# Optimization experiments

Hardware: AMD Instinct MI355X
Metric: run time of the kernel (lower is better)

Reference implementation:

```python
import jax, jax.numpy as jnp
import numpy as np

CH, G, K, STRIDE, RR = 256, 16, 7, 1, 4
GROUP = CH // G            # channels per group
PAD = (K - 1) // 2
BN_EPS = 1e-5


def setup_inputs() -> dict:
    key = jax.random.key(0)
    ks = jax.random.split(key, 9)
    b, dim = 16, 4096
    hid = CH // RR  # 64
    return {
        "x": jax.random.normal(ks[0], (b, CH, dim), jnp.float32),
        "w1": jax.random.normal(ks[1], (hid, CH), jnp.float32) * (1.0 / np.sqrt(CH)),
        "b1": jax.random.normal(ks[2], (hid,), jnp.float32) * 0.02,
        "bn_gamma": 1.0 + 0.1 * jax.random.normal(ks[3], (hid,), jnp.float32),
        "bn_beta": 0.1 * jax.random.normal(ks[4], (hid,), jnp.float32),
        "bn_mean": 0.1 * jax.random.normal(ks[5], (hid,), jnp.float32),
        "bn_var": jax.random.uniform(ks[6], (hid,), jnp.float32) + 0.5,
        "w2": jax.random.normal(ks[7], (K * G, hid), jnp.float32) * (1.0 / np.sqrt(hid)),
        "b2": jax.random.normal(ks[8], (K * G,), jnp.float32) * 0.02,
    }


def _involution(x, w1, b1, bn_gamma, bn_beta, bn_mean, bn_var, w2, b2):
    b, ch, dim = x.shape
    L = dim // STRIDE  # out_dim
    # unfold: pad then gather K shifted strided views -> [b, ch, K, L]
    xp = jnp.pad(x, ((0, 0), (0, 0), (PAD, PAD)))
    unfolded = jnp.stack(
        [xp[:, :, k : k + STRIDE * (L - 1) + 1 : STRIDE] for k in range(K)], axis=2
    )
    unfolded = unfolded.reshape(b, G, GROUP, K, L)
    # adaptive max pool to L (windows of size STRIDE); identity when STRIDE == 1
    pooled = x.reshape(b, ch, L, STRIDE).max(axis=-1)
    # kernel generator: 1x1 conv -> relu -> batchnorm (inference) -> 1x1 conv
    h = jnp.einsum("oc,bcl->bol", w1, pooled) + b1[:, None]
    h = jax.nn.relu(h)
    h = (h - bn_mean[:, None]) * jax.lax.rsqrt(bn_var[:, None] + BN_EPS)
    h = h * bn_gamma[:, None] + bn_beta[:, None]
    kern = jnp.einsum("oc,bcl->bol", w2, h) + b2[:, None]  # [b, K*G, L]
    kern = kern.reshape(b, G, K, L)
    # per-location dynamic kernel multiply + reduce over K
    out = jnp.einsum("bgkl,bgckl->bgcl", kern, unfolded)
    return out.reshape(b, ch, L)


def reference(x, w1, b1, bn_gamma, bn_beta, bn_mean, bn_var, w2, b2):
    return _involution(x, w1, b1, bn_gamma, bn_beta, bn_mean, bn_var, w2, b2)
```

## Files before the change

kernel.cpp:

```cpp
#include <hip/hip_runtime.h>

#define BB   16
#define CHN  256
#define DIMN 4096
#define KK   7
#define PADK 3
#define HID  64
#define KGN  112
#define RP   56
#define TLC  128
#define NPAN 8
#define PCH  32
#define XSTD 66
#define HSTD 132
#define BN_EPS 1e-5f

typedef __fp16 half2_t __attribute__((ext_vector_type(2)));
typedef __fp16 half8   __attribute__((ext_vector_type(8)));
typedef float  f32x4   __attribute__((ext_vector_type(4)));

union U32H2 { unsigned int u; half2_t h; };

static __device__ __forceinline__ unsigned int packf(float a, float b) {
    U32H2 t; t.h = __builtin_amdgcn_cvt_pkrtz(a, b); return t.u;
}
static __device__ __forceinline__ half2_t ash2(unsigned int u) { U32H2 t; t.u = u; return t.h; }
static __device__ __forceinline__ __fp16 u16h(unsigned short u) {
    return __builtin_bit_cast(__fp16, u);
}
static __device__ __forceinline__ unsigned short hu16(__fp16 h) {
    return __builtin_bit_cast(unsigned short, h);
}

__global__ __launch_bounds__(256) void setup_k(
    const float* __restrict__ w1, const float* __restrict__ w2,
    const float* __restrict__ bn_gamma, const float* __restrict__ bn_beta,
    const float* __restrict__ bn_mean,  const float* __restrict__ bn_var,
    __fp16* __restrict__ w1f, __fp16* __restrict__ w2f,
    float* __restrict__ scb, float* __restrict__ shb) {
    int t = blockIdx.x * 256 + threadIdx.x;
    if (t < HID * CHN) w1f[t] = (__fp16)w1[t];
    if (t < KGN * HID) w2f[t] = (__fp16)w2[t];
    if (t < HID) {
        float s = bn_gamma[t] * rsqrtf(bn_var[t] + BN_EPS);
        scb[t] = s;
        shb[t] = bn_beta[t] - bn_mean[t] * s;
    }
}

__global__ __launch_bounds__(256) void kerngen_k(
    const float* __restrict__ x,
    const __fp16* __restrict__ w1f,
    const float* __restrict__ b1,
    const float* __restrict__ scb, const float* __restrict__ shb,
    const __fp16* __restrict__ w2f,
    const float* __restrict__ b2,
    unsigned int* __restrict__ kern) {
    __shared__ unsigned int   xs[2][PCH * XSTD];
    __shared__ unsigned short hs[HID * HSTD];

    const int t    = threadIdx.x;
    const int lr   = t & 15;
    const int lg   = (t >> 4) & 3;
    const int w    = t >> 6;
    const int b    = blockIdx.x >> 5;
    const int l0   = (blockIdx.x & 31) * TLC;
    const int colw = 32 * w;

    const int colq = t & 31;
    const int chl0 = t >> 5;

    const float* xg = x + (size_t)b * CHN * DIMN + l0 + 4 * colq;

    float4 pre[4];
#pragma unroll
    for (int i = 0; i < 4; ++i)
        pre[i] = *(const float4*)(xg + (size_t)(chl0 + 8 * i) * DIMN);
#pragma unroll
    for (int i = 0; i < 4; ++i) {
        uint2 v;
        v.x = packf(pre[i].x, pre[i].y);
        v.y = packf(pre[i].z, pre[i].w);
        *(uint2*)&xs[0][(chl0 + 8 * i) * XSTD + 2 * colq] = v;
    }
    __syncthreads();

    f32x4 acc[4][2];
#pragma unroll
    for (int of = 0; of < 4; ++of)
#pragma unroll
        for (int cf = 0; cf < 2; ++cf) acc[of][cf] = (f32x4){0.f, 0.f, 0.f, 0.f};

    for (int p = 0; p < NPAN; ++p) {
        if (p + 1 < NPAN) {
#pragma unroll
            for (int i = 0; i < 4; ++i)
                pre[i] = *(const float4*)(xg + (size_t)((p + 1) * PCH + chl0 + 8 * i) * DIMN);
        }
        const unsigned short* xb16 = (const unsigned short*)xs[p & 1];
        half8 bf0, bf1;
#pragma unroll
        for (int j = 0; j < 8; ++j) {
            bf0[j] = u16h(xb16[(8 * lg + j) * HSTD + colw + lr]);
            bf1[j] = u16h(xb16[(8 * lg + j) * HSTD + colw + 16 + lr]);
        }
#pragma unroll
        for (int of = 0; of < 4; ++of) {
            half8 af = *(const half8*)(w1f + (16 * of + lr) * CHN + PCH * p + 8 * lg);
            acc[of][0] = __builtin_amdgcn_mfma_f32_16x16x32_f16(af, bf0, acc[of][0], 0, 0, 0);
            acc[of][1] = __builtin_amdgcn_mfma_f32_16x16x32_f16(af, bf1, acc[of][1], 0, 0, 0);
        }
        if (p + 1 < NPAN) {
            __syncthreads();
#pragma unroll
            for (int i = 0; i < 4; ++i) {
                uint2 v;
                v.x = packf(pre[i].x, pre[i].y);
                v.y = packf(pre[i].z, pre[i].w);
                *(uint2*)&xs[(p + 1) & 1][(chl0 + 8 * i) * XSTD + 2 * colq] = v;
            }
            __syncthreads();
        }
    }

#pragma unroll
    for (int of = 0; of < 4; ++of) {
#pragma unroll
        for (int r = 0; r < 4; ++r) {
            const int o  = 16 * of + 4 * lg + r;
            const float bo = b1[o], sc = scb[o], sh = shb[o];
#pragma unroll
            for (int cf = 0; cf < 2; ++cf) {
                float hv = fmaxf(acc[of][cf][r] + bo, 0.f) * sc + sh;
                hs[o * HSTD + colw + 16 * cf + lr] = hu16((__fp16)hv);
            }
        }
    }

    f32x4 acc2[7][2];
#pragma unroll
    for (int rf = 0; rf < 7; ++rf)
#pragma unroll
        for (int cf = 0; cf < 2; ++cf) acc2[rf][cf] = (f32x4){0.f, 0.f, 0.f, 0.f};

#pragma unroll
    for (int ks = 0; ks < 2; ++ks) {
        half8 h0, h1;
#pragma unroll
        for (int j = 0; j < 8; ++j) {
            h0[j] = u16h(hs[(32 * ks + 8 * lg + j) * HSTD + colw + lr]);
            h1[j] = u16h(hs[(32 * ks + 8 * lg + j) * HSTD + colw + 16 + lr]);
        }
#pragma unroll
        for (int rf = 0; rf < 7; ++rf) {
            half8 af = *(const half8*)(w2f + (16 * rf + lr) * HID + 32 * ks + 8 * lg);
            acc2[rf][0] = __builtin_amdgcn_mfma_f32_16x16x32_f16(af, h0, acc2[rf][0], 0, 0, 0);
            acc2[rf][1] = __builtin_amdgcn_mfma_f32_16x16x32_f16(af, h1, acc2[rf][1], 0, 0, 0);
        }
    }

    unsigned int* kb = kern + (size_t)b * RP * DIMN + l0;
#pragma unroll
    for (int rf = 0; rf < 7; ++rf) {
#pragma unroll
        for (int cf = 0; cf < 2; ++cf) {
#pragma unroll
            for (int pp = 0; pp < 2; ++pp) {
                const int r0  = 16 * rf + 4 * lg + 2 * pp;
                const int col = colw + 16 * cf + lr;
                float k0 = acc2[rf][cf][2 * pp + 0] + b2[r0 + 0];
                float k1 = acc2[rf][cf][2 * pp + 1] + b2[r0 + 1];
                kb[(size_t)(r0 >> 1) * DIMN + col] = packf(k0, k1);
            }
        }
    }
}

template <int OFF>
static __device__ inline void extract_kv(const uint4 q[4], float kv[KK][4]) {
#pragma unroll
    for (int k = 0; k < KK; ++k) {
        const int kk = k + OFF;
        const int i  = kk >> 1;
        const int h  = kk & 1;
#pragma unroll
        for (int j = 0; j < 4; ++j) {
            unsigned int u = (&q[i].x)[j];
            half2_t hh = ash2(u);
            kv[k][j] = h ? (float)hh[1] : (float)hh[0];
        }
    }
}

__global__ __launch_bounds__(256) void involution_k(
    const float* __restrict__ x,
    const unsigned int* __restrict__ kern,
    float* __restrict__ out) {
    int t  = blockIdx.x * 256 + threadIdx.x;
    int lq = t & 1023;
    int ch = (t >> 10) & 255;
    int b  = t >> 18;
    int l  = lq * 4;
    int g  = ch >> 4;

    int rbase = (7 * g) >> 1;
    const unsigned int* kb = kern + ((size_t)b * RP + rbase) * DIMN + l;
    uint4 q[4];
#pragma unroll
    for (int i = 0; i < 4; ++i) q[i] = *(const uint4*)(kb + (size_t)i * DIMN);

    float kv[KK][4];
    if (g & 1) extract_kv<1>(q, kv);
    else       extract_kv<0>(q, kv);

    const float* xrow = x + ((size_t)b * CHN + ch) * DIMN;
    float4 fa = *(const float4*)(xrow + (l > 0 ? l - 4 : 0));
    float4 fb = *(const float4*)(xrow + l);
    float4 fc = *(const float4*)(xrow + (l + 4 < DIMN ? l + 4 : DIMN - 4));

    float xr[10] = { fa.y, fa.z, fa.w, fb.x, fb.y, fb.z, fb.w, fc.x, fc.y, fc.z };
    if (l == 0)        { xr[0] = 0.f; xr[1] = 0.f; xr[2] = 0.f; }
    if (l == DIMN - 4) { xr[7] = 0.f; xr[8] = 0.f; xr[9] = 0.f; }

    float o0 = 0.f, o1 = 0.f, o2 = 0.f, o3 = 0.f;
#pragma unroll
    for (int k = 0; k < KK; ++k) {
        o0 = fmaf(kv[k][0], xr[k + 0], o0);
        o1 = fmaf(kv[k][1], xr[k + 1], o1);
        o2 = fmaf(kv[k][2], xr[k + 2], o2);
        o3 = fmaf(kv[k][3], xr[k + 3], o3);
    }
    *(float4*)(out + ((size_t)b * CHN + ch) * DIMN + l) = make_float4(o0, o1, o2, o3);
}

extern "C" void kernel_launch(void* const* d_in, const int* in_sizes, int n_in,
                              void* d_out, int out_size, void* d_ws, size_t ws_size,
                              hipStream_t stream) {
    (void)in_sizes; (void)n_in; (void)out_size; (void)ws_size;

    const float* x        = (const float*)d_in[0];
    const float* w1       = (const float*)d_in[1];
    const float* b1       = (const float*)d_in[2];
    const float* bn_gamma = (const float*)d_in[3];
    const float* bn_beta  = (const float*)d_in[4];
    const float* bn_mean  = (const float*)d_in[5];
    const float* bn_var   = (const float*)d_in[6];
    const float* w2       = (const float*)d_in[7];
    const float* b2       = (const float*)d_in[8];
    float*       out      = (float*)d_out;

    __fp16*       w1f  = (__fp16*)d_ws;
    __fp16*       w2f  = w1f + HID * CHN;
    float*        scb  = (float*)(w2f + KGN * HID);
    float*        shb  = scb + HID;
    unsigned int* kern = (unsigned int*)(shb + HID);

    setup_k<<<(HID * CHN + 255) / 256, 256, 0, stream>>>(
        w1, w2, bn_gamma, bn_beta, bn_mean, bn_var, w1f, w2f, scb, shb);
    kerngen_k<<<BB * (DIMN / TLC), 256, 0, stream>>>(
        x, w1f, b1, scb, shb, w2f, b2, kern);
    involution_k<<<(BB * CHN * (DIMN / 4)) / 256, 256, 0, stream>>>(x, kern, out);
}
```

Before: 60.02 us.

## Fuse kernel generation and involution into one kernel with LDS-resident x tile

Merges the kernel-generator GEMMs and the involution multiply-reduce into a single kernel. Each block stages a 256-channel x tile, with its 3-element halo on each side, in LDS as fp16. The generated per-location kernels also stay in LDS, so the fp16 kern buffer never goes through global memory and x is read from HBM only once instead of twice. The trade-offs are a large LDS footprint (~117KB per block), which limits residency to one block per CU and reduces latency hiding. The final multiply also now uses fp16-rounded x values instead of fp32, which reduces precision.

New measurement: 61.85 us. 3.0% more time.

```diff
diff --git a/kernel.cpp b/kernel.cpp
--- a/kernel.cpp
+++ b/kernel.cpp
@@ -7,12 +7,10 @@
 #define PADK 3
 #define HID  64
 #define KGN  112
-#define RP   56
 #define TLC  128
-#define NPAN 8
-#define PCH  32
-#define XSTD 66
-#define HSTD 132
+#define XSTD 69
+#define HSTH 138
+#define KSTD 132
 #define BN_EPS 1e-5f
 
 typedef __fp16 half2_t __attribute__((ext_vector_type(2)));
@@ -48,78 +46,92 @@
     }
 }
 
-__global__ __launch_bounds__(256) void kerngen_k(
+template <int OFF>
+static __device__ __forceinline__ void extract2(const uint2 q[4],
+                                                float kva[KK], float kvb[KK]) {
+#pragma unroll
+    for (int k = 0; k < KK; ++k) {
+        const int kk = k + OFF;
+        const int i  = kk >> 1;
+        const int h  = kk & 1;
+        half2_t a = ash2(q[i].x);
+        half2_t c = ash2(q[i].y);
+        kva[k] = h ? (float)a[1] : (float)a[0];
+        kvb[k] = h ? (float)c[1] : (float)c[0];
+    }
+}
+
+__global__ __launch_bounds__(512, 2) void fused_k(
     const float* __restrict__ x,
     const __fp16* __restrict__ w1f,
     const float* __restrict__ b1,
     const float* __restrict__ scb, const float* __restrict__ shb,
     const __fp16* __restrict__ w2f,
     const float* __restrict__ b2,
-    unsigned int* __restrict__ kern) {
-    __shared__ unsigned int   xs[2][PCH * XSTD];
-    __shared__ unsigned short hs[HID * HSTD];
+    float* __restrict__ out) {
+    __shared__ unsigned int   xs[CHN * XSTD];
+    __shared__ unsigned short hs[HID * HSTH];
+    __shared__ unsigned int   ks[56 * KSTD];
 
     const int t    = threadIdx.x;
+    const int lane = t & 63;
+    const int w    = t >> 6;
     const int lr   = t & 15;
     const int lg   = (t >> 4) & 3;
-    const int w    = t >> 6;
     const int b    = blockIdx.x >> 5;
     const int l0   = (blockIdx.x & 31) * TLC;
-    const int colw = 32 * w;
-
-    const int colq = t & 31;
-    const int chl0 = t >> 5;
-
-    const float* xg = x + (size_t)b * CHN * DIMN + l0 + 4 * colq;
-
-    float4 pre[4];
-#pragma unroll
-    for (int i = 0; i < 4; ++i)
-        pre[i] = *(const float4*)(xg + (size_t)(chl0 + 8 * i) * DIMN);
-#pragma unroll
-    for (int i = 0; i < 4; ++i) {
-        uint2 v;
-        v.x = packf(pre[i].x, pre[i].y);
-        v.y = packf(pre[i].z, pre[i].w);
-        *(uint2*)&xs[0][(chl0 + 8 * i) * XSTD + 2 * colq] = v;
+
+    unsigned short* xs16 = (unsigned short*)xs;
+
+    {
+        const int c  = t & 31;
+        const int rr = t >> 5;
+        const float* xg = x + ((size_t)b * CHN + rr) * DIMN + l0 + 4 * c;
+#pragma unroll 4
+        for (int rd = 0; rd < 16; ++rd) {
+            const int row = 16 * rd + rr;
+            float4 v = *(const float4*)(xg + (size_t)(16 * rd) * DIMN);
+            unsigned int* dst = xs + row * XSTD + 2 * c + 2;
+            dst[0] = packf(v.x, v.y);
+            dst[1] = packf(v.z, v.w);
+        }
+        const int row  = t >> 1;
+        const int side = t & 1;
+        const float* xrow = x + ((size_t)b * CHN + row) * DIMN;
+        if (side == 0) {
+#pragma unroll
+            for (int j = 0; j < 3; ++j) {
+                int dc = l0 - 3 + j;
+                float v = (dc >= 0) ? xrow[dc] : 0.0f;
+                xs16[row * (2 * XSTD) + 1 + j] = hu16((__fp16)v);
+            }
+        } else {
+#pragma unroll
+            for (int j = 0; j < 3; ++j) {
+                int dc = l0 + TLC + j;
+                float v = (dc < DIMN) ? xrow[dc] : 0.0f;
+                xs16[row * (2 * XSTD) + 132 + j] = hu16((__fp16)v);
+            }
+        }
     }
     __syncthreads();
 
-    f32x4 acc[4][2];
-#pragma unroll
-    for (int of = 0; of < 4; ++of)
-#pragma unroll
-        for (int cf = 0; cf < 2; ++cf) acc[of][cf] = (f32x4){0.f, 0.f, 0.f, 0.f};
-
-    for (int p = 0; p < NPAN; ++p) {
-        if (p + 1 < NPAN) {
-#pragma unroll
-            for (int i = 0; i < 4; ++i)
-                pre[i] = *(const float4*)(xg + (size_t)((p + 1) * PCH + chl0 + 8 * i) * DIMN);
-        }
-        const unsigned short* xb16 = (const unsigned short*)xs[p & 1];
-        half8 bf0, bf1;
-#pragma unroll
-        for (int j = 0; j < 8; ++j) {
-            bf0[j] = u16h(xb16[(8 * lg + j) * HSTD + colw + lr]);
-            bf1[j] = u16h(xb16[(8 * lg + j) * HSTD + colw + 16 + lr]);
-        }
+    const int colL = 16 * w + lr;
+
+    f32x4 acc[4];
+#pragma unroll
+    for (int of = 0; of < 4; ++of) acc[of] = (f32x4){0.f, 0.f, 0.f, 0.f};
+
+#pragma unroll
+    for (int p = 0; p < 8; ++p) {
+        half8 bf;
+#pragma unroll
+        for (int j = 0; j < 8; ++j)
+            bf[j] = u16h(xs16[(32 * p + 8 * lg + j) * (2 * XSTD) + colL + 4]);
 #pragma unroll
         for (int of = 0; of < 4; ++of) {
-            half8 af = *(const half8*)(w1f + (16 * of + lr) * CHN + PCH * p + 8 * lg);
-            acc[of][0] = __builtin_amdgcn_mfma_f32_16x16x32_f16(af, bf0, acc[of][0], 0, 0, 0);
-            acc[of][1] = __builtin_amdgcn_mfma_f32_16x16x32_f16(af, bf1, acc[of][1], 0, 0, 0);
-        }
-        if (p + 1 < NPAN) {
-            __syncthreads();
-#pragma unroll
-            for (int i = 0; i < 4; ++i) {
-                uint2 v;
-                v.x = packf(pre[i].x, pre[i].y);
-                v.y = packf(pre[i].z, pre[i].w);
-                *(uint2*)&xs[(p + 1) & 1][(chl0 + 8 * i) * XSTD + 2 * colq] = v;
-            }
-            __syncthreads();
+            half8 af = *(const half8*)(w1f + (16 * of + lr) * CHN + 32 * p + 8 * lg);
+            acc[of] = __builtin_amdgcn_mfma_f32_16x16x32_f16(af, bf, acc[of], 0, 0, 0);
         }
     }
 
@@ -127,110 +139,81 @@
     for (int of = 0; of < 4; ++of) {
 #pragma unroll
         for (int r = 0; r < 4; ++r) {
-            const int o  = 16 * of + 4 * lg + r;
-            const float bo = b1[o], sc = scb[o], sh = shb[o];
-#pragma unroll
-            for (int cf = 0; cf < 2; ++cf) {
-                float hv = fmaxf(acc[of][cf][r] + bo, 0.f) * sc + sh;
-                hs[o * HSTD + colw + 16 * cf + lr] = hu16((__fp16)hv);
-            }
-        }
-    }
-
-    f32x4 acc2[7][2];
-#pragma unroll
-    for (int rf = 0; rf < 7; ++rf)
-#pragma unroll
-        for (int cf = 0; cf < 2; ++cf) acc2[rf][cf] = (f32x4){0.f, 0.f, 0.f, 0.f};
-
-#pragma unroll
-    for (int ks = 0; ks < 2; ++ks) {
-        half8 h0, h1;
-#pragma unroll
-        for (int j = 0; j < 8; ++j) {
-            h0[j] = u16h(hs[(32 * ks + 8 * lg + j) * HSTD + colw + lr]);
-            h1[j] = u16h(hs[(32 * ks + 8 * lg + j) * HSTD + colw + 16 + lr]);
-        }
+            const int o = 16 * of + 4 * lg + r;
+            float hv = fmaxf(acc[of][r] + b1[o], 0.f) * scb[o] + shb[o];
+            hs[o * HSTH + colL] = hu16((__fp16)hv);
+        }
+    }
+
+    f32x4 acc2[7];
+#pragma unroll
+    for (int rf = 0; rf < 7; ++rf) acc2[rf] = (f32x4){0.f, 0.f, 0.f, 0.f};
+
+#pragma unroll
+    for (int kx = 0; kx < 2; ++kx) {
+        half8 bf;
+#pragma unroll
+        for (int j = 0; j < 8; ++j)
+            bf[j] = u16h(hs[(32 * kx + 8 * lg + j) * HSTH + colL]);
 #pragma unroll
         for (int rf = 0; rf < 7; ++rf) {
-            half8 af = *(const half8*)(w2f + (16 * rf + lr) * HID + 32 * ks + 8 * lg);
-            acc2[rf][0] = __builtin_amdgcn_mfma_f32_16x16x32_f16(af, h0, acc2[rf][0], 0, 0, 0);
-            acc2[rf][1] = __builtin_amdgcn_mfma_f32_16x16x32_f16(af, h1, acc2[rf][1], 0, 0, 0);
-        }
-    }
-
-    unsigned int* kb = kern + (size_t)b * RP * DIMN + l0;
+            half8 af = *(const half8*)(w2f + (16 * rf + lr) * HID + 32 * kx + 8 * lg);
+            acc2[rf] = __builtin_amdgcn_mfma_f32_16x16x32_f16(af, bf, acc2[rf], 0, 0, 0);
+        }
+    }
+
 #pragma unroll
     for (int rf = 0; rf < 7; ++rf) {
 #pragma unroll
-        for (int cf = 0; cf < 2; ++cf) {
-#pragma unroll
-            for (int pp = 0; pp < 2; ++pp) {
-                const int r0  = 16 * rf + 4 * lg + 2 * pp;
-                const int col = colw + 16 * cf + lr;
-                float k0 = acc2[rf][cf][2 * pp + 0] + b2[r0 + 0];
-                float k1 = acc2[rf][cf][2 * pp + 1] + b2[r0 + 1];
-                kb[(size_t)(r0 >> 1) * DIMN + col] = packf(k0, k1);
-            }
-        }
-    }
-}
-
-template <int OFF>
-static __device__ inline void extract_kv(const uint4 q[4], float kv[KK][4]) {
-#pragma unroll
-    for (int k = 0; k < KK; ++k) {
-        const int kk = k + OFF;
-        const int i  = kk >> 1;
-        const int h  = kk & 1;
-#pragma unroll
-        for (int j = 0; j < 4; ++j) {
-            unsigned int u = (&q[i].x)[j];
-            half2_t hh = ash2(u);
-            kv[k][j] = h ? (float)hh[1] : (float)hh[0];
-        }
-    }
-}
-
-__global__ __launch_bounds__(256) void involution_k(
-    const float* __restrict__ x,
-    const unsigned int* __restrict__ kern,
-    float* __restrict__ out) {
-    int t  = blockIdx.x * 256 + threadIdx.x;
-    int lq = t & 1023;
-    int ch = (t >> 10) & 255;
-    int b  = t >> 18;
-    int l  = lq * 4;
-    int g  = ch >> 4;
-
-    int rbase = (7 * g) >> 1;
-    const unsigned int* kb = kern + ((size_t)b * RP + rbase) * DIMN + l;
-    uint4 q[4];
-#pragma unroll
-    for (int i = 0; i < 4; ++i) q[i] = *(const uint4*)(kb + (size_t)i * DIMN);
-
-    float kv[KK][4];
-    if (g & 1) extract_kv<1>(q, kv);
-    else       extract_kv<0>(q, kv);
-
-    const float* xrow = x + ((size_t)b * CHN + ch) * DIMN;
-    float4 fa = *(const float4*)(xrow + (l > 0 ? l - 4 : 0));
-    float4 fb = *(const float4*)(xrow + l);
-    float4 fc = *(const float4*)(xrow + (l + 4 < DIMN ? l + 4 : DIMN - 4));
-
-    float xr[10] = { fa.y, fa.z, fa.w, fb.x, fb.y, fb.z, fb.w, fc.x, fc.y, fc.z };
-    if (l == 0)        { xr[0] = 0.f; xr[1] = 0.f; xr[2] = 0.f; }
-    if (l == DIMN - 4) { xr[7] = 0.f; xr[8] = 0.f; xr[9] = 0.f; }
-
-    float o0 = 0.f, o1 = 0.f, o2 = 0.f, o3 = 0.f;
-#pragma unroll
-    for (int k = 0; k < KK; ++k) {
-        o0 = fmaf(kv[k][0], xr[k + 0], o0);
-        o1 = fmaf(kv[k][1], xr[k + 1], o1);
-        o2 = fmaf(kv[k][2], xr[k + 2], o2);
-        o3 = fmaf(kv[k][3], xr[k + 3], o3);
-    }
-    *(float4*)(out + ((size_t)b * CHN + ch) * DIMN + l) = make_float4(o0, o1, o2, o3);
+        for (int p = 0; p < 2; ++p) {
+            const int r0 = 16 * rf + 4 * lg + 2 * p;
+            float k0 = acc2[rf][2 * p + 0] + b2[r0 + 0];
+            float k1 = acc2[rf][2 * p + 1] + b2[r0 + 1];
+            ks[(r0 >> 1) * KSTD + colL] = packf(k0, k1);
+        }
+    }
+    __syncthreads();
+
+    const int l  = lane;
+    const int c0 = 2 * l;
+    float* outp = out + ((size_t)b * CHN + 32 * w) * DIMN + l0 + c0;
+
+#pragma unroll
+    for (int gi = 0; gi < 2; ++gi) {
+        const int g   = 2 * w + gi;
+        const int rpb = (7 * g) >> 1;
+        uint2 q[4];
+#pragma unroll
+        for (int ii = 0; ii < 4; ++ii)
+            q[ii] = *(const uint2*)(ks + (rpb + ii) * KSTD + c0);
+        float kva[KK], kvb[KK];
+        if (gi == 0) extract2<0>(q, kva, kvb);
+        else         extract2<1>(q, kva, kvb);
+
+#pragma unroll 8
+        for (int i2 = 0; i2 < 16; ++i2) {
+            const int ch = 32 * w + 16 * gi + i2;
+            const unsigned int* xr = xs + ch * XSTD + l;
+            unsigned int uu[5];
+#pragma unroll
+            for (int j = 0; j < 5; ++j) uu[j] = xr[j];
+            float xv[8];
+#pragma unroll
+            for (int r = 1; r <= 8; ++r) {
+                unsigned int u = uu[r >> 1];
+                unsigned short us = (r & 1) ? (unsigned short)(u >> 16)
+                                            : (unsigned short)(u & 0xffff);
+                xv[r - 1] = (float)u16h(us);
+            }
+            float o0 = 0.f, o1 = 0.f;
+#pragma unroll
+            for (int k = 0; k < KK; ++k) {
+                o0 = fmaf(kva[k], xv[k],     o0);
+                o1 = fmaf(kvb[k], xv[k + 1], o1);
+            }
+            *(float2*)(outp + (size_t)(16 * gi + i2) * DIMN) = make_float2(o0, o1);
+        }
+    }
 }
 
 extern "C" void kernel_launch(void* const* d_in, const int* in_sizes, int n_in,
@@ -249,15 +232,13 @@
     const float* b2       = (const float*)d_in[8];
     float*       out      = (float*)d_out;
 
-    __fp16*       w1f  = (__fp16*)d_ws;
-    __fp16*       w2f  = w1f + HID * CHN;
-    float*        scb  = (float*)(w2f + KGN * HID);
-    float*        shb  = scb + HID;
-    unsigned int* kern = (unsigned int*)(shb + HID);
+    __fp16* w1f = (__fp16*)d_ws;
+    __fp16* w2f = w1f + HID * CHN;
+    float*  scb = (float*)(w2f + KGN * HID);
+    float*  shb = scb + HID;
 
     setup_k<<<(HID * CHN + 255) / 256, 256, 0, stream>>>(
         w1, w2, bn_gamma, bn_beta, bn_mean, bn_var, w1f, w2f, scb, shb);
-    kerngen_k<<<BB * (DIMN / TLC), 256, 0, stream>>>(
-        x, w1f, b1, scb, shb, w2f, b2, kern);
-    involution_k<<<(BB * CHN * (DIMN / 4)) / 256, 256, 0, stream>>>(x, kern, out);
-}
+    fused_k<<<BB * (DIMN / TLC), 512, 0, stream>>>(
+        x, w1f, b1, scb, shb, w2f, b2, out);
+}
```
